# Optimization experiments

Measured on AMD Instinct MI355X. Metric: run time of the kernel, lower is better.

The kernel has to match this reference:

```python
import jax, jax.numpy as jnp
import numpy as np

B, N, C, H = 8, 1025, 512, 8
G = 32  # grid size; S = G*G = N-1


def setup_inputs() -> dict:
    key = jax.random.key(0)
    ks = jax.random.split(key, 5)
    return {
        "x": jax.random.normal(ks[0], (B, N, C), dtype=jnp.float32),
        "qkv_w": jax.random.normal(ks[1], (3 * C, C), dtype=jnp.float32) * (C ** -0.5),
        "proj_w": jax.random.normal(ks[2], (C, C), dtype=jnp.float32) * (C ** -0.5),
        "proj_b": jnp.zeros((C,), dtype=jnp.float32),
        "wg_w": jax.random.normal(ks[3], (H, 64), dtype=jnp.float32) * 0.125,
        "wg_b": jnp.zeros((H,), dtype=jnp.float32),
    }


def _geometry_bias(wg_w, wg_b):
    # BoxRelationalEmbedding on a fixed 32x32 grid; batch-independent, so computed once.
    S = G * G
    xs = jnp.arange(G, dtype=jnp.float32)
    px = jnp.repeat(xs, G)   # px_min: row index per flattened cell
    py = jnp.tile(xs, G)     # py_min: col index per flattened cell
    rx0, ry0 = px / G, py / G
    rx1, ry1 = (px + 1.0) / G, (py + 1.0) / G
    cx = 0.5 * (rx0 + rx1)
    cy = 0.5 * (ry0 + ry1)
    w = rx1 - rx0 + 1.0
    h = ry1 - ry0 + 1.0
    dx = jnp.log(jnp.clip(jnp.abs((cx[:, None] - cx[None, :]) / w[:, None]), 1e-3, None))
    dy = jnp.log(jnp.clip(jnp.abs((cy[:, None] - cy[None, :]) / h[:, None]), 1e-3, None))
    dw = jnp.log(w[:, None] / w[None, :])
    dh = jnp.log(h[:, None] / h[None, :])
    pos = jnp.stack([dx, dy, dw, dh], axis=-1)  # [S,S,4]
    dim_mat = 1.0 / jnp.power(1000.0, jnp.arange(8, dtype=jnp.float32) / 8.0)  # dim_g/8 = 8 freqs
    mul = (100.0 * pos)[..., None] * dim_mat        # [S,S,4,8]
    mul = mul.reshape(S, S, 32)
    emb = jnp.concatenate([jnp.sin(mul), jnp.cos(mul)], axis=-1)  # [S,S,64]
    rgw = jax.nn.relu(jnp.einsum('ijd,hd->hij', emb, wg_w) + wg_b[:, None, None])  # [H,S,S]
    rgw = jnp.log(jnp.clip(rgw, 1e-6, None))
    # pad zero column (dim 3 cat of t1) then zero row (dim 2 cat of t2) -> [H, S+1, S+1]
    return jnp.pad(rgw, ((0, 0), (1, 0), (1, 0)))


def reference(x, qkv_w, proj_w, proj_b, wg_w, wg_b):
    b, n, c = x.shape
    hd = c // H
    scale = hd ** -0.5
    bias = _geometry_bias(wg_w, wg_b)  # [H, n, n]
    qkv = (x @ qkv_w.T).reshape(b, n, 3, H, hd)
    q, k, v = qkv[:, :, 0], qkv[:, :, 1], qkv[:, :, 2]  # each [b,n,H,hd]
    attn = jnp.einsum('bihd,bjhd->bhij', q, k) * scale + bias[None]
    attn = jax.nn.softmax(attn, axis=-1)
    out = jnp.einsum('bhij,bjhd->bihd', attn, v).reshape(b, n, c)
    return out @ proj_w.T + proj_b
```

## Files before the change

### kernel.cpp

```cpp
#include <hip/hip_runtime.h>
#include <hip/hip_bf16.h>
#include <hip/hip_fp16.h>
#include <math.h>

#define B_  8
#define N_  1025
#define C_  512
#define H_  8
#define HD_ 64
#define M_  (B_ * N_)
#define VCS 2560
#define VST 36

typedef __attribute__((ext_vector_type(8))) short short8;
typedef __attribute__((ext_vector_type(4))) float f32x4;
typedef __attribute__((ext_vector_type(4))) unsigned short us4;

__device__ inline unsigned short bf16u(float x) {
    __hip_bfloat16 t = __float2bfloat16(x);
    return *(unsigned short*)&t;
}
__device__ inline float fexp2(float x) {
    float r;
    asm("v_exp_f32 %0, %1" : "=v"(r) : "v"(x));
    return r;
}
__device__ inline float h2f(unsigned short u) {
    __half_raw hr; hr.x = u;
    return __half2float(__half(hr));
}
__device__ inline void load_lds16(const void* g, void* l) {
    __builtin_amdgcn_global_load_lds(
        (const __attribute__((address_space(1))) unsigned int*)g,
        (__attribute__((address_space(3))) unsigned int*)l, 16, 0, 0);
}

#define PER_ ((size_t)B_ * H_ * N_ * HD_)
#define SZ_QKVW (3 * C_ * C_)
#define SZ_PRJW (C_ * C_)
#define CAST_BLKS ((4198400 + 786432 + 262144) / 4 / 256)
#define EXP_BLKS 256

__global__ void prep_kernel(const float* __restrict__ x,
                            const float* __restrict__ qkv_w,
                            const float* __restrict__ proj_w,
                            const float* __restrict__ wg_w,
                            const float* __restrict__ wg_b,
                            unsigned short* __restrict__ xb,
                            unsigned short* __restrict__ wqkvb,
                            unsigned short* __restrict__ wprjb,
                            unsigned short* __restrict__ big) {
    __shared__ float tl[1024];
    int blk = blockIdx.x;
    int tid = threadIdx.x;
    if (blk < EXP_BLKS) {
        int h = blk >> 5, rs = blk & 31;
        const float* w = wg_w + h * 64;
        float wb = wg_b[h];
#pragma unroll 1
        for (int e = tid; e < 1024; e += 256) {
            int a = e >> 5, b = e & 31;
            float dx = logf(fmaxf((float)a * (1.0f / 33.0f), 0.001f));
            float dy = logf(fmaxf((float)b * (1.0f / 33.0f), 0.001f));
            float acc = wb;
#pragma unroll
            for (int k = 0; k < 8; k++) {
                float f = powf(1000.0f, -(float)k * 0.125f);
                float X = 100.0f * dx * f;
                float Y = 100.0f * dy * f;
                acc += w[k]      * sinf(X);
                acc += w[8 + k]  * sinf(Y);
                acc += w[32 + k] * cosf(X);
                acc += w[40 + k] * cosf(Y);
                acc += w[48 + k] + w[56 + k];
            }
            tl[e] = log2f(fmaxf(fmaxf(acc, 0.0f), 1e-6f));
        }
        __syncthreads();
        int rbase = rs * 36;
#pragma unroll 1
        for (int e8 = tid; e8 < 36 * 132; e8 += 256) {
            int rr = e8 / 132;
            int cg = e8 - rr * 132;
            int r = rbase + rr;
            int c0 = cg * 8;
            int i = min(r, 1024) - 1;
            int ix = i >> 5, iy = i & 31;
            unsigned short o8[8];
#pragma unroll
            for (int e = 0; e < 8; e++) {
                int c = c0 + e;
                float v;
                if (r == 0 || c == 0) v = 0.f;
                else if (c > 1024)    v = -60000.f;
                else {
                    int j = c - 1;
                    int da = __sad(ix, j >> 5, 0u);
                    int db = __sad(iy, j & 31, 0u);
                    v = tl[da * 32 + db];
                }
                __half hv = __float2half(v);
                o8[e] = *(unsigned short*)&hv;
            }
            *(short8*)(big + ((size_t)h * 1152 + r) * 1056 + c0) = *(short8*)o8;
        }
        return;
    }
    long i4 = ((long)(blk - EXP_BLKS) * 256 + tid) * 4;
    const float* src;
    unsigned short* dst;
    long off;
    if (i4 < (long)PER_)                    { src = x;      dst = xb;    off = i4; }
    else if (i4 < (long)PER_ + SZ_QKVW)     { src = qkv_w;  dst = wqkvb; off = i4 - PER_; }
    else                                    { src = proj_w; dst = wprjb; off = i4 - PER_ - SZ_QKVW; }
    float4 v = *(const float4*)(src + off);
    ushort4 p;
    p.x = bf16u(v.x); p.y = bf16u(v.y); p.z = bf16u(v.z); p.w = bf16u(v.w);
    *(ushort4*)(dst + off) = p;
}

#define GK 512

__global__ __launch_bounds__(256) void gemm_qkv_mfma(
        const unsigned short* __restrict__ A, const unsigned short* __restrict__ W,
        unsigned short* __restrict__ qb, unsigned short* __restrict__ kb,
        unsigned short* __restrict__ vtc) {
    __shared__ __align__(16) unsigned short As[128 * 32];
    __shared__ __align__(16) unsigned short Bs[128 * 32];
    int tid = threadIdx.x;
    int w = tid >> 6, lane = tid & 63;
    int quad = lane >> 4, l16 = lane & 15;
    int m0 = blockIdx.y * 128;
    int n0 = blockIdx.x * 128;
    int wr = (w >> 1) * 64, wc = (w & 1) * 64;

    int c0 = tid, c1 = tid + 256;
    int a_r0 = min(m0 + (c0 >> 2), M_ - 1), a_c0 = (c0 & 3) * 8;
    int a_r1 = min(m0 + (c1 >> 2), M_ - 1), a_c1 = (c1 & 3) * 8;
    int b_r0 = n0 + (c0 >> 2), b_r1 = n0 + (c1 >> 2);

    int which = n0 >> 9;
    int h = ((n0 + wc) >> 6) & 7;

    f32x4 acc[4][4];
    const f32x4 zero4 = {0.f, 0.f, 0.f, 0.f};
#pragma unroll
    for (int mi = 0; mi < 4; mi++)
#pragma unroll
        for (int ni = 0; ni < 4; ni++) acc[mi][ni] = zero4;

    for (int k0 = 0; k0 < GK; k0 += 32) {
        __syncthreads();
        load_lds16(A + (size_t)a_r0 * GK + k0 + a_c0, &As[w * 512]);
        load_lds16(A + (size_t)a_r1 * GK + k0 + a_c1, &As[2048 + w * 512]);
        load_lds16(W + (size_t)b_r0 * GK + k0 + a_c0, &Bs[w * 512]);
        load_lds16(W + (size_t)b_r1 * GK + k0 + a_c1, &Bs[2048 + w * 512]);
        __syncthreads();
        short8 af[4], bf[4];
#pragma unroll
        for (int mi = 0; mi < 4; mi++)
            af[mi] = *(const short8*)&As[(wr + mi * 16 + l16) * 32 + quad * 8];
#pragma unroll
        for (int ni = 0; ni < 4; ni++)
            bf[ni] = *(const short8*)&Bs[(wc + ni * 16 + l16) * 32 + quad * 8];
#pragma unroll
        for (int mi = 0; mi < 4; mi++)
#pragma unroll
            for (int ni = 0; ni < 4; ni++)
                acc[mi][ni] = __builtin_amdgcn_mfma_f32_16x16x32_bf16(
                    bf[ni], af[mi], acc[mi][ni], 0, 0, 0);
    }

    if (which < 2) {
        unsigned short* dst = (which == 0) ? qb : kb;
        float sc = (which == 0) ? 0.18033688f : 1.0f;
#pragma unroll
        for (int mi = 0; mi < 4; mi++) {
            int m = m0 + wr + mi * 16 + l16;
            if (m < M_) {
                int bb = m / N_;
                int i  = m - bb * N_;
                unsigned short* row = dst + ((size_t)(bb * H_ + h) * N_ + i) * HD_;
#pragma unroll
                for (int ni = 0; ni < 4; ni++) {
                    ushort4 pk;
                    pk.x = bf16u(acc[mi][ni][0] * sc);
                    pk.y = bf16u(acc[mi][ni][1] * sc);
                    pk.z = bf16u(acc[mi][ni][2] * sc);
                    pk.w = bf16u(acc[mi][ni][3] * sc);
                    *(ushort4*)(row + ni * 16 + quad * 4) = pk;
                }
            }
        }
    } else {
#pragma unroll
        for (int mi = 0; mi < 4; mi++) {
            int m = m0 + wr + mi * 16 + l16;
            if (m < M_) {
                int bb = m / N_;
                int i  = m - bb * N_;
                int ch = i >> 5, key = i & 31;
                int slot = ((key >> 2) & 3) * 8 + ((key >> 4) << 2) + (key & 3);
                unsigned short* base = vtc + ((size_t)(bb * H_ + h) * VST + ch) * VCS + slot;
#pragma unroll
                for (int ni = 0; ni < 4; ni++)
#pragma unroll
                    for (int reg = 0; reg < 4; reg++)
                        base[(ni * 16 + quad * 4 + reg) * 40] = bf16u(acc[mi][ni][reg]);
            }
        }
    }
}

__global__ __launch_bounds__(256) void gemm_proj_mfma(
        const unsigned short* __restrict__ A, const unsigned short* __restrict__ W,
        const float* __restrict__ bias, float* __restrict__ out) {
    __shared__ __align__(16) unsigned short As[128 * 32];
    __shared__ __align__(16) unsigned short Bs[128 * 32];
    int tid = threadIdx.x;
    int w = tid >> 6, lane = tid & 63;
    int quad = lane >> 4, l16 = lane & 15;
    int m0 = blockIdx.y * 128;
    int n0 = blockIdx.x * 128;
    int wr = (w >> 1) * 64, wc = (w & 1) * 64;

    int c0 = tid, c1 = tid + 256;
    int a_r0 = min(m0 + (c0 >> 2), M_ - 1), a_c0 = (c0 & 3) * 8;
    int a_r1 = min(m0 + (c1 >> 2), M_ - 1), a_c1 = (c1 & 3) * 8;
    int b_r0 = n0 + (c0 >> 2), b_r1 = n0 + (c1 >> 2);

    f32x4 acc[4][4];
    const f32x4 zero4 = {0.f, 0.f, 0.f, 0.f};
#pragma unroll
    for (int mi = 0; mi < 4; mi++)
#pragma unroll
        for (int ni = 0; ni < 4; ni++) acc[mi][ni] = zero4;

    for (int k0 = 0; k0 < GK; k0 += 32) {
        __syncthreads();
        load_lds16(A + (size_t)a_r0 * GK + k0 + a_c0, &As[w * 512]);
        load_lds16(A + (size_t)a_r1 * GK + k0 + a_c1, &As[2048 + w * 512]);
        load_lds16(W + (size_t)b_r0 * GK + k0 + a_c0, &Bs[w * 512]);
        load_lds16(W + (size_t)b_r1 * GK + k0 + a_c1, &Bs[2048 + w * 512]);
        __syncthreads();
        short8 af[4], bf[4];
#pragma unroll
        for (int mi = 0; mi < 4; mi++)
            af[mi] = *(const short8*)&As[(wr + mi * 16 + l16) * 32 + quad * 8];
#pragma unroll
        for (int ni = 0; ni < 4; ni++)
            bf[ni] = *(const short8*)&Bs[(wc + ni * 16 + l16) * 32 + quad * 8];
#pragma unroll
        for (int mi = 0; mi < 4; mi++)
#pragma unroll
            for (int ni = 0; ni < 4; ni++)
                acc[mi][ni] = __builtin_amdgcn_mfma_f32_16x16x32_bf16(
                    af[mi], bf[ni], acc[mi][ni], 0, 0, 0);
    }

    float bvals[4];
#pragma unroll
    for (int ni = 0; ni < 4; ni++) bvals[ni] = bias[n0 + wc + ni * 16 + l16];
#pragma unroll
    for (int mi = 0; mi < 4; mi++)
#pragma unroll
        for (int reg = 0; reg < 4; reg++) {
            int m = m0 + wr + mi * 16 + quad * 4 + reg;
            if (m < M_) {
                float* row = out + (size_t)m * C_ + n0 + wc;
#pragma unroll
                for (int ni = 0; ni < 4; ni++)
                    row[ni * 16 + l16] = acc[mi][ni][reg] + bvals[ni];
            }
        }
}

#define RT_ 288

__global__ __launch_bounds__(576, 3) void attn_fused(
        const unsigned short* __restrict__ qg,
        const unsigned short* __restrict__ kg,
        const unsigned short* __restrict__ vtc,
        const unsigned short* __restrict__ bigtab,
        unsigned short* __restrict__ ob) {
    __shared__ __align__(16) unsigned short Ks[2][6144];
    __shared__ __align__(16) unsigned short Vs[2][7680];

    int tid = threadIdx.x;
    int w = tid >> 6, lane = tid & 63;
    int quad = lane >> 4, l16 = lane & 15;

    int lin = blockIdx.x;
    int bh = lin & 63;
    int mt = lin >> 6;
    int b = bh >> 3, h = bh & 7;

    const unsigned short* qp = qg + (size_t)bh * N_ * HD_;
    const unsigned short* kp = kg + (size_t)bh * N_ * HD_;
    const unsigned short* vp = vtc + (size_t)bh * VST * VCS;

    int qrA = mt * RT_ + w * 32 + l16;
    const unsigned short* btA = bigtab + ((size_t)h * 1152 + qrA) * 1056 + quad * 4;
    const unsigned short* btB = btA + (size_t)16 * 1056;

    short8 qfA[2], qfB[2];
    {
        int rowA = min(qrA, N_ - 1);
        int rowB = min(qrA + 16, N_ - 1);
        qfA[0] = *(const short8*)(qp + (size_t)rowA * HD_ + quad * 8);
        qfA[1] = *(const short8*)(qp + (size_t)rowA * HD_ + 32 + quad * 8);
        qfB[0] = *(const short8*)(qp + (size_t)rowB * HD_ + quad * 8);
        qfB[1] = *(const short8*)(qp + (size_t)rowB * HD_ + 32 + quad * 8);
    }

    f32x4 oA[4], oB[4], lA, lB;
    const f32x4 zero4 = {0.f, 0.f, 0.f, 0.f};
#pragma unroll
    for (int g2 = 0; g2 < 4; g2++) { oA[g2] = zero4; oB[g2] = zero4; }
    lA = zero4; lB = zero4;
    short8 ones;
    {
        short one_bf = (short)0x3F80;
#pragma unroll
        for (int j = 0; j < 8; j++) ones[j] = one_bf;
    }

    auto stage = [&](int t, int buf) {
#pragma unroll
        for (int r2 = 0; r2 < 3; r2++) {
            int cb = w * 3 + r2;
            if (cb < 12) {
                int ch = cb * 64 + lane;
                int ct = ch >> 7, rem = ch & 127;
                int oct = rem >> 4, k16 = rem & 15;
                int key = min(t * 96 + ct * 16 + k16, N_ - 1);
                load_lds16(kp + (size_t)key * HD_ + oct * 8, &Ks[buf][cb * 512]);
            } else {
                int vb = cb - 12;
                load_lds16(vp + (size_t)t * 3 * VCS + (size_t)(vb * 64 + lane) * 8,
                           &Vs[buf][vb * 512]);
            }
        }
    };

    us4 bAc[6], bAn[6];
#pragma unroll
    for (int i = 0; i < 6; i++)
        bAn[i] = *(const us4*)(btA + (i >> 1) * 32 + (i & 1) * 16);
    stage(0, 0);

#pragma unroll 1
    for (int t = 0; t < 11; t++) {
        int buf = t & 1;
        __syncthreads();

#pragma unroll
        for (int i = 0; i < 6; i++) bAc[i] = bAn[i];
        us4 bB[6];
        {
            const unsigned short* btp = btB + t * 96;
#pragma unroll
            for (int i = 0; i < 6; i++)
                bB[i] = *(const us4*)(btp + (i >> 1) * 32 + (i & 1) * 16);
        }
        if (t < 10) {
            const unsigned short* btp = btA + (t + 1) * 96;
#pragma unroll
            for (int i = 0; i < 6; i++)
                bAn[i] = *(const us4*)(btp + (i >> 1) * 32 + (i & 1) * 16);
            stage(t + 1, buf ^ 1);
        }

#pragma unroll
        for (int ks = 0; ks < 3; ks++) {
            f32x4 sA[2], sB[2];
#pragma unroll
            for (int ctl = 0; ctl < 2; ctl++) {
                int ct = ks * 2 + ctl;
                short8 kf0 = *(const short8*)&Ks[buf][(ct * 128 + quad * 16 + l16) * 8];
                short8 kf1 = *(const short8*)&Ks[buf][(ct * 128 + (4 + quad) * 16 + l16) * 8];
                sA[ctl] = __builtin_amdgcn_mfma_f32_16x16x32_bf16(kf0, qfA[0], zero4, 0, 0, 0);
                sA[ctl] = __builtin_amdgcn_mfma_f32_16x16x32_bf16(kf1, qfA[1], sA[ctl], 0, 0, 0);
                sB[ctl] = __builtin_amdgcn_mfma_f32_16x16x32_bf16(kf0, qfB[0], zero4, 0, 0, 0);
                sB[ctl] = __builtin_amdgcn_mfma_f32_16x16x32_bf16(kf1, qfB[1], sB[ctl], 0, 0, 0);
            }
            const unsigned short* vcp = &Vs[buf][ks * 2560 + quad * 8];
            short8 vf[4];
#pragma unroll
            for (int g2 = 0; g2 < 4; g2++)
                vf[g2] = *(const short8*)(vcp + (g2 * 16 + l16) * 40);

            short8 pfA;
#pragma unroll
            for (int e = 0; e < 8; e++) {
                int par = e >> 2, r = e & 3;
                float bia = h2f(bAc[ks * 2 + par][r]);
                pfA[e] = (short)bf16u(fexp2(sA[par][r] + bia));
            }
            __builtin_amdgcn_s_setprio(1);
#pragma unroll
            for (int g2 = 0; g2 < 4; g2++)
                oA[g2] = __builtin_amdgcn_mfma_f32_16x16x32_bf16(pfA, vf[g2], oA[g2], 0, 0, 0);
            lA = __builtin_amdgcn_mfma_f32_16x16x32_bf16(pfA, ones, lA, 0, 0, 0);
            __builtin_amdgcn_s_setprio(0);

            short8 pfB;
#pragma unroll
            for (int e = 0; e < 8; e++) {
                int par = e >> 2, r = e & 3;
                float bia = h2f(bB[ks * 2 + par][r]);
                pfB[e] = (short)bf16u(fexp2(sB[par][r] + bia));
            }
            __builtin_amdgcn_s_setprio(1);
#pragma unroll
            for (int g2 = 0; g2 < 4; g2++)
                oB[g2] = __builtin_amdgcn_mfma_f32_16x16x32_bf16(pfB, vf[g2], oB[g2], 0, 0, 0);
            lB = __builtin_amdgcn_mfma_f32_16x16x32_bf16(pfB, ones, lB, 0, 0, 0);
            __builtin_amdgcn_s_setprio(0);
        }
    }

#pragma unroll
    for (int grp = 0; grp < 2; grp++) {
        int rbase = mt * RT_ + w * 32 + grp * 16 + quad * 4;
        const f32x4* oX = grp ? oB : oA;
        const f32x4& lX = grp ? lB : lA;
#pragma unroll
        for (int reg = 0; reg < 4; reg++) {
            int r = rbase + reg;
            if (r < N_) {
                float inv = 1.0f / lX[reg];
                unsigned short* orow = ob + ((size_t)b * N_ + r) * C_ + h * HD_ + l16;
#pragma unroll
                for (int g2 = 0; g2 < 4; g2++)
                    orow[g2 * 16] = bf16u(oX[g2][reg] * inv);
            }
        }
    }
}

extern "C" void kernel_launch(void* const* d_in, const int* in_sizes, int n_in,
                              void* d_out, int out_size, void* d_ws, size_t ws_size,
                              hipStream_t stream) {
    const float* x      = (const float*)d_in[0];
    const float* qkv_w  = (const float*)d_in[1];
    const float* proj_w = (const float*)d_in[2];
    const float* proj_b = (const float*)d_in[3];
    const float* wg_w   = (const float*)d_in[4];
    const float* wg_b   = (const float*)d_in[5];
    float* out = (float*)d_out;

    const size_t per = PER_;
    char* ws = (char*)d_ws;
    unsigned short* bigtab = (unsigned short*)ws;
    unsigned short* xb     = bigtab + (size_t)8 * 1152 * 1056;
    unsigned short* wqkvb  = xb + per;
    unsigned short* wprjb  = wqkvb + (size_t)SZ_QKVW;
    unsigned short* qb     = wprjb + (size_t)SZ_PRJW;
    unsigned short* kb     = qb + per;
    unsigned short* vtc    = kb + per;
    unsigned short* ob     = vtc + (size_t)64 * VST * VCS;

    prep_kernel<<<EXP_BLKS + CAST_BLKS, 256, 0, stream>>>(x, qkv_w, proj_w, wg_w, wg_b,
                                                          xb, wqkvb, wprjb, bigtab);
    gemm_qkv_mfma<<<dim3(12, 65), 256, 0, stream>>>(xb, wqkvb, qb, kb, vtc);
    attn_fused<<<256, 576, 0, stream>>>(qb, kb, vtc, bigtab, ob);
    gemm_proj_mfma<<<dim3(4, 65), 256, 0, stream>>>(ob, wprjb, proj_b, out);
}
```

Measured before the change: 185.2 us.

## Double-buffer LDS tiles in both GEMMs and tabulate geometry sin/cos

Both bf16 MFMA GEMMs (QKV and output projection) now use two LDS buffers per operand. The next K-slice is issued into the alternate buffer before the current slice is computed, which removes one barrier per iteration and lets global-to-LDS loads overlap with MFMA work. The geometry-bias prep now precomputes the sin/cos values for the 32 offsets and 8 frequencies once into shared tables. It also hoists the constant weight tail sum instead of calling powf, sinf and cosf per element. The cost is twice the LDS per GEMM block, which may lower occupancy.

Result: no change. 182.2 us (-1.6%).

```diff
diff --git a/kernel.cpp b/kernel.cpp
--- a/kernel.cpp
+++ b/kernel.cpp
@@ -51,28 +51,36 @@
                             unsigned short* __restrict__ wprjb,
                             unsigned short* __restrict__ big) {
     __shared__ float tl[1024];
+    __shared__ float sT[256], cT[256];
     int blk = blockIdx.x;
     int tid = threadIdx.x;
     if (blk < EXP_BLKS) {
         int h = blk >> 5, rs = blk & 31;
         const float* w = wg_w + h * 64;
+        if (tid < 256) {
+            const float fr[8] = {1.0f, 0.421696503f, 0.177827941f, 0.074989421f,
+                                 0.031622777f, 0.013335214f, 0.005623413f, 0.002371374f};
+            int a = tid >> 3, k = tid & 7;
+            float dxv = logf(fmaxf((float)a * (1.0f / 33.0f), 0.001f));
+            float ang = 100.0f * dxv * fr[k];
+            sT[tid] = sinf(ang);
+            cT[tid] = cosf(ang);
+        }
+        __syncthreads();
         float wb = wg_b[h];
+        float wtail = 0.f;
+#pragma unroll
+        for (int k = 0; k < 8; k++) wtail += w[48 + k] + w[56 + k];
 #pragma unroll 1
         for (int e = tid; e < 1024; e += 256) {
             int a = e >> 5, b = e & 31;
-            float dx = logf(fmaxf((float)a * (1.0f / 33.0f), 0.001f));
-            float dy = logf(fmaxf((float)b * (1.0f / 33.0f), 0.001f));
-            float acc = wb;
+            float acc = wb + wtail;
 #pragma unroll
             for (int k = 0; k < 8; k++) {
-                float f = powf(1000.0f, -(float)k * 0.125f);
-                float X = 100.0f * dx * f;
-                float Y = 100.0f * dy * f;
-                acc += w[k]      * sinf(X);
-                acc += w[8 + k]  * sinf(Y);
-                acc += w[32 + k] * cosf(X);
-                acc += w[40 + k] * cosf(Y);
-                acc += w[48 + k] + w[56 + k];
+                acc += w[k]      * sT[a * 8 + k];
+                acc += w[8 + k]  * sT[b * 8 + k];
+                acc += w[32 + k] * cT[a * 8 + k];
+                acc += w[40 + k] * cT[b * 8 + k];
             }
             tl[e] = log2f(fmaxf(fmaxf(acc, 0.0f), 1e-6f));
         }
@@ -125,8 +133,8 @@
         const unsigned short* __restrict__ A, const unsigned short* __restrict__ W,
         unsigned short* __restrict__ qb, unsigned short* __restrict__ kb,
         unsigned short* __restrict__ vtc) {
-    __shared__ __align__(16) unsigned short As[128 * 32];
-    __shared__ __align__(16) unsigned short Bs[128 * 32];
+    __shared__ __align__(16) unsigned short As[2][128 * 32];
+    __shared__ __align__(16) unsigned short Bs[2][128 * 32];
     int tid = threadIdx.x;
     int w = tid >> 6, lane = tid & 63;
     int quad = lane >> 4, l16 = lane & 15;
@@ -149,20 +157,25 @@
 #pragma unroll
         for (int ni = 0; ni < 4; ni++) acc[mi][ni] = zero4;
 
+    auto stage = [&](int k0, int buf) {
+        load_lds16(A + (size_t)a_r0 * GK + k0 + a_c0, &As[buf][w * 512]);
+        load_lds16(A + (size_t)a_r1 * GK + k0 + a_c1, &As[buf][2048 + w * 512]);
+        load_lds16(W + (size_t)b_r0 * GK + k0 + a_c0, &Bs[buf][w * 512]);
+        load_lds16(W + (size_t)b_r1 * GK + k0 + a_c1, &Bs[buf][2048 + w * 512]);
+    };
+    stage(0, 0);
+
     for (int k0 = 0; k0 < GK; k0 += 32) {
+        int buf = (k0 >> 5) & 1;
         __syncthreads();
-        load_lds16(A + (size_t)a_r0 * GK + k0 + a_c0, &As[w * 512]);
-        load_lds16(A + (size_t)a_r1 * GK + k0 + a_c1, &As[2048 + w * 512]);
-        load_lds16(W + (size_t)b_r0 * GK + k0 + a_c0, &Bs[w * 512]);
-        load_lds16(W + (size_t)b_r1 * GK + k0 + a_c1, &Bs[2048 + w * 512]);
-        __syncthreads();
+        if (k0 + 32 < GK) stage(k0 + 32, buf ^ 1);
         short8 af[4], bf[4];
 #pragma unroll
         for (int mi = 0; mi < 4; mi++)
-            af[mi] = *(const short8*)&As[(wr + mi * 16 + l16) * 32 + quad * 8];
+            af[mi] = *(const short8*)&As[buf][(wr + mi * 16 + l16) * 32 + quad * 8];
 #pragma unroll
         for (int ni = 0; ni < 4; ni++)
-            bf[ni] = *(const short8*)&Bs[(wc + ni * 16 + l16) * 32 + quad * 8];
+            bf[ni] = *(const short8*)&Bs[buf][(wc + ni * 16 + l16) * 32 + quad * 8];
 #pragma unroll
         for (int mi = 0; mi < 4; mi++)
 #pragma unroll
@@ -215,8 +228,8 @@
 __global__ __launch_bounds__(256) void gemm_proj_mfma(
         const unsigned short* __restrict__ A, const unsigned short* __restrict__ W,
         const float* __restrict__ bias, float* __restrict__ out) {
-    __shared__ __align__(16) unsigned short As[128 * 32];
-    __shared__ __align__(16) unsigned short Bs[128 * 32];
+    __shared__ __align__(16) unsigned short As[2][128 * 32];
+    __shared__ __align__(16) unsigned short Bs[2][128 * 32];
     int tid = threadIdx.x;
     int w = tid >> 6, lane = tid & 63;
     int quad = lane >> 4, l16 = lane & 15;
@@ -236,20 +249,25 @@
 #pragma unroll
         for (int ni = 0; ni < 4; ni++) acc[mi][ni] = zero4;
 
+    auto stage = [&](int k0, int buf) {
+        load_lds16(A + (size_t)a_r0 * GK + k0 + a_c0, &As[buf][w * 512]);
+        load_lds16(A + (size_t)a_r1 * GK + k0 + a_c1, &As[buf][2048 + w * 512]);
+        load_lds16(W + (size_t)b_r0 * GK + k0 + a_c0, &Bs[buf][w * 512]);
+        load_lds16(W + (size_t)b_r1 * GK + k0 + a_c1, &Bs[buf][2048 + w * 512]);
+    };
+    stage(0, 0);
+
     for (int k0 = 0; k0 < GK; k0 += 32) {
+        int buf = (k0 >> 5) & 1;
         __syncthreads();
-        load_lds16(A + (size_t)a_r0 * GK + k0 + a_c0, &As[w * 512]);
-        load_lds16(A + (size_t)a_r1 * GK + k0 + a_c1, &As[2048 + w * 512]);
-        load_lds16(W + (size_t)b_r0 * GK + k0 + a_c0, &Bs[w * 512]);
-        load_lds16(W + (size_t)b_r1 * GK + k0 + a_c1, &Bs[2048 + w * 512]);
-        __syncthreads();
+        if (k0 + 32 < GK) stage(k0 + 32, buf ^ 1);
         short8 af[4], bf[4];
 #pragma unroll
         for (int mi = 0; mi < 4; mi++)
-            af[mi] = *(const short8*)&As[(wr + mi * 16 + l16) * 32 + quad * 8];
+            af[mi] = *(const short8*)&As[buf][(wr + mi * 16 + l16) * 32 + quad * 8];
 #pragma unroll
         for (int ni = 0; ni < 4; ni++)
-            bf[ni] = *(const short8*)&Bs[(wc + ni * 16 + l16) * 32 + quad * 8];
+            bf[ni] = *(const short8*)&Bs[buf][(wc + ni * 16 + l16) * 32 + quad * 8];
 #pragma unroll
         for (int mi = 0; mi < 4; mi++)
 #pragma unroll
```
